# Optimization experiments

Hardware: AMD Instinct MI355X
Metric: run time of the kernel (lower is better)

## Reference

```python
import jax, jax.numpy as jnp
import numpy as np

B, N, C_IN = 8, 2048, 3
D = 64            # graph-conv feature dim
SPARSE_K = 8      # k_neighbors(16) * sparse_ratio(0.5)
LEVELS = 3        # wavelet_levels
H1, H2 = 256, 128 # fusion hidden dims

def _lin(key, fan_in, fan_out):
    k1, k2 = jax.random.split(key)
    s = 1.0 / np.sqrt(fan_in)
    W = jax.random.uniform(k1, (fan_in, fan_out), minval=-s, maxval=s, dtype=jnp.float32)
    b = jax.random.uniform(k2, (fan_out,), minval=-s, maxval=s, dtype=jnp.float32)
    return W, b

def setup_inputs() -> dict:
    key = jax.random.key(0)
    ks = jax.random.split(key, 12)
    x = jax.random.normal(ks[0], (B, N, C_IN), dtype=jnp.float32)
    W1, b1 = _lin(ks[1], C_IN, D)          # feature_transform
    W2, b2 = _lin(ks[2], 2 * D, D)         # edge_conv
    Ws1, bs1 = _lin(ks[3], C_IN, 64)       # suppressor layer 1
    Ws2, bs2 = _lin(ks[4], 64, LEVELS)     # suppressor layer 2
    Wf1, bf1 = _lin(ks[5], D * LEVELS, H1) # fusion
    Wf2, bf2 = _lin(ks[6], H1, H2)
    Wf3, bf3 = _lin(ks[7], H2, C_IN)
    ones = jnp.ones; zeros = jnp.zeros
    return {
        'x': x,
        'W1': W1, 'b1': b1, 'g1': ones((D,), jnp.float32), 'be1': zeros((D,), jnp.float32),
        'W2': W2, 'b2': b2, 'g2': ones((D,), jnp.float32), 'be2': zeros((D,), jnp.float32),
        'Ws1': Ws1, 'bs1': bs1, 'Ws2': Ws2, 'bs2': bs2,
        'Wf1': Wf1, 'bf1': bf1, 'gf1': ones((H1,), jnp.float32), 'bef1': zeros((H1,), jnp.float32),
        'Wf2': Wf2, 'bf2': bf2, 'gf2': ones((H2,), jnp.float32), 'bef2': zeros((H2,), jnp.float32),
        'Wf3': Wf3, 'bf3': bf3,
    }

def _leaky(v):
    return jnp.where(v > 0, v, 0.2 * v)

def reference(x, W1, b1, g1, be1, W2, b2, g2, be2, Ws1, bs1, Ws2, bs2,
              Wf1, bf1, gf1, bef1, Wf2, bf2, gf2, bef2, Wf3, bf3):
    # ---- AdaptiveSparseGraphConv ----
    # feature transform + eval-mode BN (running mean 0 / var 1 -> affine)
    feat = _leaky((x @ W1 + b1) * g1 + be1)                     # [B,N,D]
    # KNN via squared distances (monotonic in true cdist)
    x2 = jnp.sum(x * x, axis=-1)                                # [B,N]
    d2 = x2[:, :, None] + x2[:, None, :] - 2.0 * jnp.einsum('bnc,bmc->bnm', x, x)
    _, idx = jax.lax.top_k(-d2, SPARSE_K)                       # [B,N,k] nearest
    neighbor = jax.vmap(lambda f, i: f[i])(feat, idx)           # [B,N,k,D]
    edge = jnp.concatenate(
        [jnp.broadcast_to(feat[:, :, None, :], neighbor.shape), neighbor], axis=-1)  # [B,N,k,2D]
    conv = _leaky((edge @ W2 + b2) * g2 + be2)                  # [B,N,k,D]
    agg = jnp.max(conv, axis=2)                                 # [B,N,D]
    # ---- AdaptiveFrequencySupressor (per-point wavelet-level weights) ----
    fw = jax.nn.sigmoid(jax.nn.relu(x @ Ws1 + bs1) @ Ws2 + bs2) # [B,N,LEVELS]
    # frequency-adaptive multi-level weighting, concat across levels
    multi = (agg[:, :, None, :] * fw[:, :, :, None]).reshape(B, N, LEVELS * D)  # [B,N,LEVELS*D]
    # ---- EnhancedMultiScaleFusion (eval: dropout off, BN affine) ----
    h = _leaky((multi @ Wf1 + bf1) * gf1 + bef1)
    h = _leaky((h @ Wf2 + bf2) * gf2 + bef2)
    delta = h @ Wf3 + bf3                                       # [B,N,3]
    # ---- residual regularized output ----
    return x + 0.1 * delta
```

## Files before the change

### kernel.cpp

```cpp
#include <hip/hip_runtime.h>
#include <hip/hip_bf16.h>
#include <math.h>

#define BB   8
#define NN   2048
#define BN   16384
#define KNB  8

__device__ __forceinline__ float leaky(float v){ return v > 0.f ? v : 0.2f*v; }

__device__ __forceinline__ ushort f2bf(float f){
    unsigned u = __float_as_uint(f);
    return (ushort)((u + 0x7FFFu + ((u >> 16) & 1u)) >> 16);
}
__device__ __forceinline__ float bf2f(ushort h){
    return __uint_as_float(((unsigned)h) << 16);
}

using bf16x8 = __attribute__((ext_vector_type(8))) short;
using f32x16 = __attribute__((ext_vector_type(16))) float;

__global__ __launch_bounds__(256) void k_pq(
    const float* __restrict__ x,
    const float* __restrict__ W1, const float* __restrict__ b1,
    const float* __restrict__ g1, const float* __restrict__ be1,
    const float* __restrict__ W2,
    const float* __restrict__ Wf1, const float* __restrict__ Wf2,
    float* __restrict__ P, ushort* __restrict__ Qb,
    ushort* __restrict__ Wf1T, ushort* __restrict__ Wf2T)
{
    int t = threadIdx.x;
    int bid = blockIdx.x;
    if (bid >= 256) {
        if (bid < 280) {
            int base = (bid - 256) * 2048 + t * 8;
            #pragma unroll
            for (int j = 0; j < 8; ++j) {
                int e = base + j;
                int n = e / 192, k = e % 192;
                Wf1T[e] = f2bf(Wf1[k*256 + n]);
            }
        } else {
            int base = (bid - 280) * 2048 + t * 8;
            #pragma unroll
            for (int j = 0; j < 8; ++j) {
                int e = base + j;
                int n = e / 256, k = e % 256;
                Wf2T[e] = f2bf(Wf2[k*128 + n]);
            }
        }
        return;
    }

    __shared__ float F_s[64*66];
    __shared__ float W_s[32*132];

    int rb = bid * 64;

    {
        int d = t & 63, g = t >> 6;
        float w0 = W1[d], w1 = W1[64+d], w2 = W1[128+d];
        float bb = b1[d], gg = g1[d], ee = be1[d];
        #pragma unroll 4
        for (int i = 0; i < 16; ++i) {
            int r = g*16 + i;
            const float* xp = &x[(rb + r)*3];
            float f = xp[0]*w0 + xp[1]*w1 + xp[2]*w2 + bb;
            f = leaky(f*gg + ee);
            F_s[r*66 + d] = f;
        }
    }

    int tx = t & 15, ty = t >> 4;
    float acc[4][8];
    #pragma unroll
    for (int i = 0; i < 4; ++i)
        #pragma unroll
        for (int j = 0; j < 8; ++j) acc[i][j] = 0.f;

    for (int k0 = 0; k0 < 64; k0 += 32) {
        __syncthreads();
        #pragma unroll
        for (int it = 0; it < 2; ++it) {
            int i2 = t + it*256;
            int k = i2 >> 4, c8 = (i2 & 15) * 8;
            const float* src = &W2[(k0 + k + (c8 >= 64 ? 64 : 0))*64 + (c8 & 63)];
            *(float4*)&W_s[k*132 + c8]     = *(const float4*)src;
            *(float4*)&W_s[k*132 + c8 + 4] = *(const float4*)(src + 4);
        }
        __syncthreads();
        #pragma unroll 4
        for (int kk = 0; kk < 32; ++kk) {
            float a[4];
            #pragma unroll
            for (int i = 0; i < 4; ++i) a[i] = F_s[(ty*4 + i)*66 + k0 + kk];
            float4 wA = *(const float4*)&W_s[kk*132 + tx*8];
            float4 wB = *(const float4*)&W_s[kk*132 + tx*8 + 4];
            #pragma unroll
            for (int i = 0; i < 4; ++i) {
                acc[i][0] = fmaf(a[i], wA.x, acc[i][0]);
                acc[i][1] = fmaf(a[i], wA.y, acc[i][1]);
                acc[i][2] = fmaf(a[i], wA.z, acc[i][2]);
                acc[i][3] = fmaf(a[i], wA.w, acc[i][3]);
                acc[i][4] = fmaf(a[i], wB.x, acc[i][4]);
                acc[i][5] = fmaf(a[i], wB.y, acc[i][5]);
                acc[i][6] = fmaf(a[i], wB.z, acc[i][6]);
                acc[i][7] = fmaf(a[i], wB.w, acc[i][7]);
            }
        }
    }

    #pragma unroll
    for (int i = 0; i < 4; ++i) {
        int r = rb + ty*4 + i;
        if (tx < 8) {
            *(float4*)&P[r*64 + tx*8]     = make_float4(acc[i][0], acc[i][1], acc[i][2], acc[i][3]);
            *(float4*)&P[r*64 + tx*8 + 4] = make_float4(acc[i][4], acc[i][5], acc[i][6], acc[i][7]);
        } else {
            union { ushort u[8]; uint4 v; } pk;
            #pragma unroll
            for (int j = 0; j < 8; ++j) pk.u[j] = f2bf(acc[i][j]);
            *(uint4*)&Qb[r*64 + (tx - 8)*8] = pk.v;
        }
    }
}

#define CEF(a, b) { float mn_ = fminf(a,b), mx_ = fmaxf(a,b); (a) = mn_; (b) = mx_; }

__global__ __launch_bounds__(1024, 8) void k_knn(const float* __restrict__ x, int* __restrict__ idxo)
{
    __shared__ __align__(16) char smem[51584];
    float4* sp    = (float4*)smem;
    float*  mg    = (float*) (smem + 32768);
    float*  v8buf = (float*) (smem + 49152);
    int*    eqbuf = (int*)   (smem + 49280);
    int*    cnt   = (int*)   (smem + 51328);
    int*    ecnt  = (int*)   (smem + 51456);

    int t = threadIdx.x;
    int b = blockIdx.x >> 6;
    int qbase = (blockIdx.x & 63) * 32;
    int q = t & 31, seg = t >> 5;
    int w = t >> 6, lane = t & 63;

    for (int i = t; i < NN; i += 1024) {
        float a = x[(b*NN + i)*3 + 0];
        float c = x[(b*NN + i)*3 + 1];
        float e = x[(b*NN + i)*3 + 2];
        sp[i] = make_float4(a, c, e, a*a + c*c + e*e);
    }
    __syncthreads();

    float4 qv = sp[qbase + q];
    float R[8];
    #pragma unroll
    for (int j = 0; j < 8; ++j) R[j] = 1e30f;

    int m0 = seg * 64;
    #pragma unroll 2
    for (int g = 0; g < 8; ++g) {
        float S[8];
        #pragma unroll
        for (int jj = 0; jj < 8; ++jj) {
            int m = m0 + g*8 + jj;
            float4 v = sp[m];
            float s = qv.x*v.x; s = fmaf(qv.y, v.y, s); s = fmaf(qv.z, v.z, s);
            float d2 = fmaf(-2.f, s, qv.w + v.w);
            S[jj] = fmaxf(d2, 0.f);
        }
        CEF(S[0],S[1]); CEF(S[2],S[3]); CEF(S[4],S[5]); CEF(S[6],S[7]);
        CEF(S[0],S[2]); CEF(S[1],S[3]); CEF(S[4],S[6]); CEF(S[5],S[7]);
        CEF(S[1],S[2]); CEF(S[5],S[6]);
        CEF(S[0],S[4]); CEF(S[1],S[5]); CEF(S[2],S[6]); CEF(S[3],S[7]);
        CEF(S[2],S[4]); CEF(S[3],S[5]);
        CEF(S[1],S[2]); CEF(S[3],S[4]); CEF(S[5],S[6]);
        #pragma unroll
        for (int j = 0; j < 8; ++j) R[j] = fminf(R[j], S[7-j]);
        CEF(R[0],R[4]); CEF(R[1],R[5]); CEF(R[2],R[6]); CEF(R[3],R[7]);
        CEF(R[0],R[2]); CEF(R[1],R[3]); CEF(R[4],R[6]); CEF(R[5],R[7]);
        CEF(R[0],R[1]); CEF(R[2],R[3]); CEF(R[4],R[5]); CEF(R[6],R[7]);
    }

    {
        float Rp[8];
        #pragma unroll
        for (int j = 0; j < 8; ++j) Rp[j] = __shfl_xor(R[j], 32, 64);
        float C[8];
        #pragma unroll
        for (int j = 0; j < 8; ++j) C[j] = fminf(R[j], Rp[7-j]);
        CEF(C[0],C[4]); CEF(C[1],C[5]); CEF(C[2],C[6]); CEF(C[3],C[7]);
        CEF(C[0],C[2]); CEF(C[1],C[3]); CEF(C[4],C[6]); CEF(C[5],C[7]);
        CEF(C[0],C[1]); CEF(C[2],C[3]); CEF(C[4],C[5]); CEF(C[6],C[7]);
        if (lane < 32) {
            #pragma unroll
            for (int j = 0; j < 8; ++j) mg[(w*32 + lane)*8 + j] = C[j];
        }
    }

    #pragma unroll
    for (int lvl = 0; lvl < 4; ++lvl) {
        int P = 8 >> lvl;
        int sh = 3 - lvl;
        bool active = (t < 32*P);
        float C[8];
        int qq = 0, p = 0;
        __syncthreads();
        if (active) {
            qq = t >> sh; p = t & (P - 1);
            float A[8], Bv[8];
            #pragma unroll
            for (int j = 0; j < 8; ++j) {
                A[j]  = mg[((2*p)*32 + qq)*8 + j];
                Bv[j] = mg[((2*p + 1)*32 + qq)*8 + j];
            }
            #pragma unroll
            for (int j = 0; j < 8; ++j) C[j] = fminf(A[j], Bv[7-j]);
            CEF(C[0],C[4]); CEF(C[1],C[5]); CEF(C[2],C[6]); CEF(C[3],C[7]);
            CEF(C[0],C[2]); CEF(C[1],C[3]); CEF(C[4],C[6]); CEF(C[5],C[7]);
            CEF(C[0],C[1]); CEF(C[2],C[3]); CEF(C[4],C[5]); CEF(C[6],C[7]);
        }
        __syncthreads();
        if (active) {
            if (P > 1) {
                #pragma unroll
                for (int j = 0; j < 8; ++j) mg[(p*32 + qq)*8 + j] = C[j];
            } else {
                v8buf[qq] = C[7];
            }
        }
    }
    if (t >= 32 && t < 64)  cnt[t - 32] = 0;
    if (t >= 64 && t < 96)  ecnt[t - 64] = 0;
    __syncthreads();

    {
        float v8 = v8buf[q];
        int obase = (b*NN + qbase + q)*KNB;
        #pragma unroll 4
        for (int jj = 0; jj < 64; ++jj) {
            int m = m0 + jj;
            float4 v = sp[m];
            float s = qv.x*v.x; s = fmaf(qv.y, v.y, s); s = fmaf(qv.z, v.z, s);
            float d2 = fmaf(-2.f, s, qv.w + v.w);
            d2 = fmaxf(d2, 0.f);
            if (d2 <= v8) {
                if (d2 < v8) {
                    int slot = atomicAdd(&cnt[q], 1);
                    idxo[obase + slot] = b*NN + m;
                } else {
                    int slot = atomicAdd(&ecnt[q], 1);
                    if (slot < 16) eqbuf[q*16 + slot] = m;
                }
            }
        }
    }
    __syncthreads();

    if (t < 32) {
        int qq = t;
        int cLT = cnt[qq];
        int ne = ecnt[qq]; if (ne > 16) ne = 16;
        int need = 8 - cLT;
        int obase = (b*NN + qbase + qq)*KNB;
        for (int k = 0; k < need; ++k) {
            int best = 0x7FFFFFFF, bi = -1;
            for (int i = 0; i < ne; ++i) {
                int v = eqbuf[qq*16 + i];
                if (v < best) { best = v; bi = i; }
            }
            if (bi >= 0) {
                eqbuf[qq*16 + bi] = 0x7FFFFFFF;
                idxo[obase + cLT + k] = b*NN + best;
            }
        }
    }
}

__global__ __launch_bounds__(256) void k_fuse(
    const float* __restrict__ x,
    const float* __restrict__ P, const ushort* __restrict__ Qb,
    const int* __restrict__ idx,
    const float* __restrict__ Ws1, const float* __restrict__ bs1,
    const float* __restrict__ Ws2, const float* __restrict__ bs2,
    const float* __restrict__ b2, const float* __restrict__ g2,
    const float* __restrict__ be2,
    const ushort* __restrict__ Wf1T, const float* __restrict__ bf1,
    const float* __restrict__ gf1, const float* __restrict__ bef1,
    const ushort* __restrict__ Wf2T, const float* __restrict__ bf2,
    const float* __restrict__ gf2, const float* __restrict__ bef2,
    const float* __restrict__ Wf3, const float* __restrict__ bf3,
    float* __restrict__ out)
{
    __shared__ __align__(16) char smem[60928];
    ushort* A_s  = (ushort*)smem;
    ushort* B_s  = (ushort*)(smem + 25600);
    ushort* h1_s = (ushort*)smem;
    ushort* B2_s = (ushort*)(smem + 40960);
    float*  pd   = (float*) (smem + 59392);

    int t = threadIdx.x, w = t >> 6, lane = t & 63;
    int rb = blockIdx.x * 64;

    {
        float ws1a = Ws1[lane], ws1b = Ws1[64+lane], ws1c = Ws1[128+lane];
        float bs1v = bs1[lane];
        float ws2a = Ws2[lane*3+0], ws2b = Ws2[lane*3+1], ws2c = Ws2[lane*3+2];
        float bs20 = bs2[0], bs21 = bs2[1], bs22 = bs2[2];
        float g2v = g2[lane], be2v = be2[lane], b2v = b2[lane];
        for (int i = 0; i < 16; ++i) {
            int r = w*16 + i, p = rb + r;
            float x0 = x[p*3+0], x1 = x[p*3+1], x2 = x[p*3+2];
            float h = fmaxf(fmaf(x2, ws1c, fmaf(x1, ws1b, fmaf(x0, ws1a, bs1v))), 0.f);
            float s0 = h*ws2a, s1 = h*ws2b, s2 = h*ws2c;
            #pragma unroll
            for (int off = 32; off; off >>= 1) {
                s0 += __shfl_xor(s0, off, 64);
                s1 += __shfl_xor(s1, off, 64);
                s2 += __shfl_xor(s2, off, 64);
            }
            float fw0 = 1.f/(1.f + expf(-(s0 + bs20)));
            float fw1 = 1.f/(1.f + expf(-(s1 + bs21)));
            float fw2 = 1.f/(1.f + expf(-(s2 + bs22)));
            float Pv = P[p*64 + lane] + b2v;
            float mx = -1e30f;
            #pragma unroll
            for (int j = 0; j < KNB; ++j) {
                int nb = idx[p*KNB + j];
                float qv = bf2f(Qb[nb*64 + lane]);
                mx = fmaxf(mx, leaky((Pv + qv)*g2v + be2v));
            }
            A_s[r*200 + lane]       = f2bf(mx * fw0);
            A_s[r*200 + 64 + lane]  = f2bf(mx * fw1);
            A_s[r*200 + 128 + lane] = f2bf(mx * fw2);
        }
    }

    int rg = w >> 1;
    int nh = (w & 1) * 128;
    int l31 = lane & 31, kb = (lane >> 5) * 8;
    int row = rg*32 + l31;

    f32x16 acc[4];
    #pragma unroll
    for (int n2 = 0; n2 < 4; ++n2)
        #pragma unroll
        for (int i = 0; i < 16; ++i) acc[n2][i] = 0.f;

    for (int k0 = 0; k0 < 192; k0 += 64) {
        __syncthreads();
        #pragma unroll
        for (int it = 0; it < 8; ++it) {
            int i = t + it*256;
            int n = i >> 3, kq = (i & 7)*8;
            *(uint4*)&B_s[n*72 + kq] = *(const uint4*)&Wf1T[n*192 + k0 + kq];
        }
        __syncthreads();
        #pragma unroll
        for (int s = 0; s < 4; ++s) {
            bf16x8 a = *(const bf16x8*)&A_s[row*200 + k0 + s*16 + kb];
            #pragma unroll
            for (int n2 = 0; n2 < 4; ++n2) {
                bf16x8 b = *(const bf16x8*)&B_s[(nh + n2*32 + l31)*72 + s*16 + kb];
                acc[n2] = __builtin_amdgcn_mfma_f32_32x32x16_bf16(a, b, acc[n2], 0, 0, 0);
            }
        }
    }
    __syncthreads();

    #pragma unroll
    for (int n2 = 0; n2 < 4; ++n2) {
        int c = nh + n2*32 + l31;
        float bv = bf1[c], gv = gf1[c], ev = bef1[c];
        #pragma unroll
        for (int r16 = 0; r16 < 16; ++r16) {
            int rr = (r16 & 3) + 8*(r16 >> 2) + 4*(lane >> 5);
            float v = leaky((acc[n2][r16] + bv)*gv + ev);
            h1_s[(rg*32 + rr)*264 + c] = f2bf(v);
        }
    }

    int ch = (w & 1) * 64;
    f32x16 acc2[2];
    #pragma unroll
    for (int n2 = 0; n2 < 2; ++n2)
        #pragma unroll
        for (int i = 0; i < 16; ++i) acc2[n2][i] = 0.f;

    for (int k0 = 0; k0 < 256; k0 += 64) {
        __syncthreads();
        #pragma unroll
        for (int it = 0; it < 4; ++it) {
            int i = t + it*256;
            int n = i >> 3, kq = (i & 7)*8;
            *(uint4*)&B2_s[n*72 + kq] = *(const uint4*)&Wf2T[n*256 + k0 + kq];
        }
        __syncthreads();
        #pragma unroll
        for (int s = 0; s < 4; ++s) {
            bf16x8 a = *(const bf16x8*)&h1_s[row*264 + k0 + s*16 + kb];
            #pragma unroll
            for (int n2 = 0; n2 < 2; ++n2) {
                bf16x8 b = *(const bf16x8*)&B2_s[(ch + n2*32 + l31)*72 + s*16 + kb];
                acc2[n2] = __builtin_amdgcn_mfma_f32_32x32x16_bf16(a, b, acc2[n2], 0, 0, 0);
            }
        }
    }

    float bv[2], gv[2], ev[2], w3[2][3];
    #pragma unroll
    for (int n2 = 0; n2 < 2; ++n2) {
        int c = ch + n2*32 + l31;
        bv[n2] = bf2[c]; gv[n2] = gf2[c]; ev[n2] = bef2[c];
        #pragma unroll
        for (int l = 0; l < 3; ++l) w3[n2][l] = Wf3[c*3 + l];
    }
    __syncthreads();
    #pragma unroll
    for (int r16 = 0; r16 < 16; ++r16) {
        float d0 = 0.f, d1 = 0.f, d2 = 0.f;
        #pragma unroll
        for (int n2 = 0; n2 < 2; ++n2) {
            float v = leaky((acc2[n2][r16] + bv[n2])*gv[n2] + ev[n2]);
            d0 = fmaf(v, w3[n2][0], d0);
            d1 = fmaf(v, w3[n2][1], d1);
            d2 = fmaf(v, w3[n2][2], d2);
        }
        #pragma unroll
        for (int off = 16; off; off >>= 1) {
            d0 += __shfl_xor(d0, off, 64);
            d1 += __shfl_xor(d1, off, 64);
            d2 += __shfl_xor(d2, off, 64);
        }
        int rr = rg*32 + (r16 & 3) + 8*(r16 >> 2) + 4*(lane >> 5);
        if (l31 < 3) {
            float dl = (l31 == 0) ? d0 : (l31 == 1 ? d1 : d2);
            pd[(rr*2 + (w & 1))*3 + l31] = dl;
        }
    }
    __syncthreads();

    if (t < 192) {
        int r = t / 3, l = t - r*3;
        float delta = pd[(r*2 + 0)*3 + l] + pd[(r*2 + 1)*3 + l] + bf3[l];
        out[(rb + r)*3 + l] = x[(rb + r)*3 + l] + 0.1f*delta;
    }
}

extern "C" void kernel_launch(void* const* d_in, const int* in_sizes, int n_in,
                              void* d_out, int out_size, void* d_ws, size_t ws_size,
                              hipStream_t stream)
{
    const float* x    = (const float*)d_in[0];
    const float* W1   = (const float*)d_in[1];
    const float* b1   = (const float*)d_in[2];
    const float* g1   = (const float*)d_in[3];
    const float* be1  = (const float*)d_in[4];
    const float* W2   = (const float*)d_in[5];
    const float* b2   = (const float*)d_in[6];
    const float* g2   = (const float*)d_in[7];
    const float* be2  = (const float*)d_in[8];
    const float* Ws1  = (const float*)d_in[9];
    const float* bs1  = (const float*)d_in[10];
    const float* Ws2  = (const float*)d_in[11];
    const float* bs2  = (const float*)d_in[12];
    const float* Wf1  = (const float*)d_in[13];
    const float* bf1  = (const float*)d_in[14];
    const float* gf1  = (const float*)d_in[15];
    const float* bef1 = (const float*)d_in[16];
    const float* Wf2  = (const float*)d_in[17];
    const float* bf2  = (const float*)d_in[18];
    const float* gf2  = (const float*)d_in[19];
    const float* bef2 = (const float*)d_in[20];
    const float* Wf3  = (const float*)d_in[21];
    const float* bf3  = (const float*)d_in[22];
    float* out = (float*)d_out;

    char* ws = (char*)d_ws;
    int*    idx   = (int*)   (ws + 0);
    ushort* Wf1T  = (ushort*)(ws + (1u << 20));
    ushort* Wf2T  = (ushort*)(ws + (1u << 20) + (512u << 10));
    float*  P     = (float*) (ws + (2u  << 20));
    ushort* Qb    = (ushort*)(ws + (6u  << 20));

    k_pq<<<296, 256, 0, stream>>>(x, W1, b1, g1, be1, W2, Wf1, Wf2, P, Qb, Wf1T, Wf2T);
    k_knn<<<BB*64, 1024, 0, stream>>>(x, idx);
    k_fuse<<<BN/64, 256, 0, stream>>>(x, P, Qb, idx, Ws1, bs1, Ws2, bs2, b2, g2, be2,
                                      Wf1T, bf1, gf1, bef1, Wf2T, bf2, gf2, bef2,
                                      Wf3, bf3, out);
}
```

Baseline: 163.2 us.

## Merge projection and KNN kernels, shrink fuse tiles to 16 rows with direct-global MFMA

The P/Q projection, weight-transpose and KNN kernels become one 1024-thread launch, with block index ranges selecting the role, so one launch and the gap between the first two stages go away. The fuse kernel now handles 16 rows per block instead of 64, using 16x16x32 MFMAs that read the transposed weights straight from global memory (relying on cache) instead of staging them in shared memory. This cuts LDS use from about 60KB to 9KB and quadruples the block count to raise occupancy. It also prefetches neighbor indices and gathered Q values before the per-point max. The cost is more repeated global and L2 weight traffic and smaller MFMA tiles.

Measured after the change: 157.7 us. 3.3% less time.

```diff
diff --git a/kernel.cpp b/kernel.cpp
--- a/kernel.cpp
+++ b/kernel.cpp
@@ -1,5 +1,4 @@
 #include <hip/hip_runtime.h>
-#include <hip/hip_bf16.h>
 #include <math.h>
 
 #define BB   8
@@ -18,22 +17,87 @@
 }
 
 using bf16x8 = __attribute__((ext_vector_type(8))) short;
-using f32x16 = __attribute__((ext_vector_type(16))) float;
-
-__global__ __launch_bounds__(256) void k_pq(
+using f32x4  = __attribute__((ext_vector_type(4)))  float;
+
+#define CEF(a, b) { float mn_ = fminf(a,b), mx_ = fmaxf(a,b); (a) = mn_; (b) = mx_; }
+
+__global__ __launch_bounds__(1024, 8) void k_front(
     const float* __restrict__ x,
     const float* __restrict__ W1, const float* __restrict__ b1,
     const float* __restrict__ g1, const float* __restrict__ be1,
     const float* __restrict__ W2,
     const float* __restrict__ Wf1, const float* __restrict__ Wf2,
     float* __restrict__ P, ushort* __restrict__ Qb,
-    ushort* __restrict__ Wf1T, ushort* __restrict__ Wf2T)
+    ushort* __restrict__ Wf1T, ushort* __restrict__ Wf2T,
+    int* __restrict__ idxo)
 {
+    __shared__ __align__(16) char smem[51584];
     int t = threadIdx.x;
     int bid = blockIdx.x;
-    if (bid >= 256) {
-        if (bid < 280) {
-            int base = (bid - 256) * 2048 + t * 8;
+
+    if (bid < 256) {
+        float* F_s = (float*)smem;
+        float* W_s = (float*)(smem + 16896);
+        int rb = bid * 64;
+
+        {
+            int d = t & 63, g = t >> 6;
+            float w0 = W1[d], w1 = W1[64+d], w2 = W1[128+d];
+            float bb = b1[d], gg = g1[d], ee = be1[d];
+            #pragma unroll
+            for (int i = 0; i < 4; ++i) {
+                int r = g*4 + i;
+                const float* xp = &x[(rb + r)*3];
+                float f = xp[0]*w0 + xp[1]*w1 + xp[2]*w2 + bb;
+                F_s[r*66 + d] = leaky(f*gg + ee);
+            }
+        }
+
+        int tx = t & 15, ty = t >> 4;
+        float acc[8];
+        #pragma unroll
+        for (int j = 0; j < 8; ++j) acc[j] = 0.f;
+
+        for (int k0 = 0; k0 < 64; k0 += 32) {
+            __syncthreads();
+            {
+                int k = t >> 5, c4 = (t & 31) * 4;
+                const float* src = &W2[(k0 + k + (c4 >= 64 ? 64 : 0))*64 + (c4 & 63)];
+                *(float4*)&W_s[k*132 + c4] = *(const float4*)src;
+            }
+            __syncthreads();
+            #pragma unroll 8
+            for (int kk = 0; kk < 32; ++kk) {
+                float a = F_s[ty*66 + k0 + kk];
+                float4 wA = *(const float4*)&W_s[kk*132 + tx*8];
+                float4 wB = *(const float4*)&W_s[kk*132 + tx*8 + 4];
+                acc[0] = fmaf(a, wA.x, acc[0]);
+                acc[1] = fmaf(a, wA.y, acc[1]);
+                acc[2] = fmaf(a, wA.z, acc[2]);
+                acc[3] = fmaf(a, wA.w, acc[3]);
+                acc[4] = fmaf(a, wB.x, acc[4]);
+                acc[5] = fmaf(a, wB.y, acc[5]);
+                acc[6] = fmaf(a, wB.z, acc[6]);
+                acc[7] = fmaf(a, wB.w, acc[7]);
+            }
+        }
+
+        int r = rb + ty;
+        if (tx < 8) {
+            *(float4*)&P[r*64 + tx*8]     = make_float4(acc[0], acc[1], acc[2], acc[3]);
+            *(float4*)&P[r*64 + tx*8 + 4] = make_float4(acc[4], acc[5], acc[6], acc[7]);
+        } else {
+            union { ushort u[8]; uint4 v; } pk;
+            #pragma unroll
+            for (int j = 0; j < 8; ++j) pk.u[j] = f2bf(acc[j]);
+            *(uint4*)&Qb[r*64 + (tx - 8)*8] = pk.v;
+        }
+        return;
+    }
+
+    if (bid < 266) {
+        if (bid < 262) {
+            int base = (bid - 256) * 8192 + t * 8;
             #pragma unroll
             for (int j = 0; j < 8; ++j) {
                 int e = base + j;
@@ -41,95 +105,17 @@
                 Wf1T[e] = f2bf(Wf1[k*256 + n]);
             }
         } else {
-            int base = (bid - 280) * 2048 + t * 8;
+            int base = (bid - 262) * 8192 + t * 8;
             #pragma unroll
             for (int j = 0; j < 8; ++j) {
                 int e = base + j;
-                int n = e / 256, k = e % 256;
+                int n = e >> 8, k = e & 255;
                 Wf2T[e] = f2bf(Wf2[k*128 + n]);
             }
         }
         return;
     }
 
-    __shared__ float F_s[64*66];
-    __shared__ float W_s[32*132];
-
-    int rb = bid * 64;
-
-    {
-        int d = t & 63, g = t >> 6;
-        float w0 = W1[d], w1 = W1[64+d], w2 = W1[128+d];
-        float bb = b1[d], gg = g1[d], ee = be1[d];
-        #pragma unroll 4
-        for (int i = 0; i < 16; ++i) {
-            int r = g*16 + i;
-            const float* xp = &x[(rb + r)*3];
-            float f = xp[0]*w0 + xp[1]*w1 + xp[2]*w2 + bb;
-            f = leaky(f*gg + ee);
-            F_s[r*66 + d] = f;
-        }
-    }
-
-    int tx = t & 15, ty = t >> 4;
-    float acc[4][8];
-    #pragma unroll
-    for (int i = 0; i < 4; ++i)
-        #pragma unroll
-        for (int j = 0; j < 8; ++j) acc[i][j] = 0.f;
-
-    for (int k0 = 0; k0 < 64; k0 += 32) {
-        __syncthreads();
-        #pragma unroll
-        for (int it = 0; it < 2; ++it) {
-            int i2 = t + it*256;
-            int k = i2 >> 4, c8 = (i2 & 15) * 8;
-            const float* src = &W2[(k0 + k + (c8 >= 64 ? 64 : 0))*64 + (c8 & 63)];
-            *(float4*)&W_s[k*132 + c8]     = *(const float4*)src;
-            *(float4*)&W_s[k*132 + c8 + 4] = *(const float4*)(src + 4);
-        }
-        __syncthreads();
-        #pragma unroll 4
-        for (int kk = 0; kk < 32; ++kk) {
-            float a[4];
-            #pragma unroll
-            for (int i = 0; i < 4; ++i) a[i] = F_s[(ty*4 + i)*66 + k0 + kk];
-            float4 wA = *(const float4*)&W_s[kk*132 + tx*8];
-            float4 wB = *(const float4*)&W_s[kk*132 + tx*8 + 4];
-            #pragma unroll
-            for (int i = 0; i < 4; ++i) {
-                acc[i][0] = fmaf(a[i], wA.x, acc[i][0]);
-                acc[i][1] = fmaf(a[i], wA.y, acc[i][1]);
-                acc[i][2] = fmaf(a[i], wA.z, acc[i][2]);
-                acc[i][3] = fmaf(a[i], wA.w, acc[i][3]);
-                acc[i][4] = fmaf(a[i], wB.x, acc[i][4]);
-                acc[i][5] = fmaf(a[i], wB.y, acc[i][5]);
-                acc[i][6] = fmaf(a[i], wB.z, acc[i][6]);
-                acc[i][7] = fmaf(a[i], wB.w, acc[i][7]);
-            }
-        }
-    }
-
-    #pragma unroll
-    for (int i = 0; i < 4; ++i) {
-        int r = rb + ty*4 + i;
-        if (tx < 8) {
-            *(float4*)&P[r*64 + tx*8]     = make_float4(acc[i][0], acc[i][1], acc[i][2], acc[i][3]);
-            *(float4*)&P[r*64 + tx*8 + 4] = make_float4(acc[i][4], acc[i][5], acc[i][6], acc[i][7]);
-        } else {
-            union { ushort u[8]; uint4 v; } pk;
-            #pragma unroll
-            for (int j = 0; j < 8; ++j) pk.u[j] = f2bf(acc[i][j]);
-            *(uint4*)&Qb[r*64 + (tx - 8)*8] = pk.v;
-        }
-    }
-}
-
-#define CEF(a, b) { float mn_ = fminf(a,b), mx_ = fmaxf(a,b); (a) = mn_; (b) = mx_; }
-
-__global__ __launch_bounds__(1024, 8) void k_knn(const float* __restrict__ x, int* __restrict__ idxo)
-{
-    __shared__ __align__(16) char smem[51584];
     float4* sp    = (float4*)smem;
     float*  mg    = (float*) (smem + 32768);
     float*  v8buf = (float*) (smem + 49152);
@@ -137,9 +123,9 @@
     int*    cnt   = (int*)   (smem + 51328);
     int*    ecnt  = (int*)   (smem + 51456);
 
-    int t = threadIdx.x;
-    int b = blockIdx.x >> 6;
-    int qbase = (blockIdx.x & 63) * 32;
+    int kbid = bid - 266;
+    int b = kbid >> 6;
+    int qbase = (kbid & 63) * 32;
     int q = t & 31, seg = t >> 5;
     int w = t >> 6, lane = t & 63;
 
@@ -199,14 +185,14 @@
 
     #pragma unroll
     for (int lvl = 0; lvl < 4; ++lvl) {
-        int P = 8 >> lvl;
+        int Pn = 8 >> lvl;
         int sh = 3 - lvl;
-        bool active = (t < 32*P);
+        bool active = (t < 32*Pn);
         float C[8];
         int qq = 0, p = 0;
         __syncthreads();
         if (active) {
-            qq = t >> sh; p = t & (P - 1);
+            qq = t >> sh; p = t & (Pn - 1);
             float A[8], Bv[8];
             #pragma unroll
             for (int j = 0; j < 8; ++j) {
@@ -221,7 +207,7 @@
         }
         __syncthreads();
         if (active) {
-            if (P > 1) {
+            if (Pn > 1) {
                 #pragma unroll
                 for (int j = 0; j < 8; ++j) mg[(p*32 + qq)*8 + j] = C[j];
             } else {
@@ -276,7 +262,7 @@
     }
 }
 
-__global__ __launch_bounds__(256) void k_fuse(
+__global__ __launch_bounds__(256, 4) void k_fuse(
     const float* __restrict__ x,
     const float* __restrict__ P, const ushort* __restrict__ Qb,
     const int* __restrict__ idx,
@@ -291,15 +277,14 @@
     const float* __restrict__ Wf3, const float* __restrict__ bf3,
     float* __restrict__ out)
 {
-    __shared__ __align__(16) char smem[60928];
+    __shared__ __align__(16) char smem[9216];
     ushort* A_s  = (ushort*)smem;
-    ushort* B_s  = (ushort*)(smem + 25600);
     ushort* h1_s = (ushort*)smem;
-    ushort* B2_s = (ushort*)(smem + 40960);
-    float*  pd   = (float*) (smem + 59392);
+    float*  pd   = (float*) (smem + 8448);
 
     int t = threadIdx.x, w = t >> 6, lane = t & 63;
-    int rb = blockIdx.x * 64;
+    int rb = blockIdx.x * 16;
+    int l15 = lane & 15, kg = lane >> 4, kb = kg * 8;
 
     {
         float ws1a = Ws1[lane], ws1b = Ws1[64+lane], ws1c = Ws1[128+lane];
@@ -307,8 +292,21 @@
         float ws2a = Ws2[lane*3+0], ws2b = Ws2[lane*3+1], ws2c = Ws2[lane*3+2];
         float bs20 = bs2[0], bs21 = bs2[1], bs22 = bs2[2];
         float g2v = g2[lane], be2v = be2[lane], b2v = b2[lane];
-        for (int i = 0; i < 16; ++i) {
-            int r = w*16 + i, p = rb + r;
+
+        int p0 = rb + w*4;
+        float Pv[4]; int nb[4][8];
+        #pragma unroll
+        for (int i = 0; i < 4; ++i) {
+            Pv[i] = P[(p0 + i)*64 + lane] + b2v;
+            #pragma unroll
+            for (int j = 0; j < 8; ++j) nb[i][j] = idx[(p0 + i)*8 + j];
+        }
+        #pragma unroll
+        for (int i = 0; i < 4; ++i) {
+            int p = p0 + i;
+            float qg[8];
+            #pragma unroll
+            for (int j = 0; j < 8; ++j) qg[j] = bf2f(Qb[nb[i][j]*64 + lane]);
             float x0 = x[p*3+0], x1 = x[p*3+1], x2 = x[p*3+2];
             float h = fmaxf(fmaf(x2, ws1c, fmaf(x1, ws1b, fmaf(x0, ws1a, bs1v))), 0.f);
             float s0 = h*ws2a, s1 = h*ws2b, s2 = h*ws2c;
@@ -321,47 +319,33 @@
             float fw0 = 1.f/(1.f + expf(-(s0 + bs20)));
             float fw1 = 1.f/(1.f + expf(-(s1 + bs21)));
             float fw2 = 1.f/(1.f + expf(-(s2 + bs22)));
-            float Pv = P[p*64 + lane] + b2v;
             float mx = -1e30f;
             #pragma unroll
-            for (int j = 0; j < KNB; ++j) {
-                int nb = idx[p*KNB + j];
-                float qv = bf2f(Qb[nb*64 + lane]);
-                mx = fmaxf(mx, leaky((Pv + qv)*g2v + be2v));
-            }
+            for (int j = 0; j < 8; ++j)
+                mx = fmaxf(mx, leaky((Pv[i] + qg[j])*g2v + be2v));
+            int r = w*4 + i;
             A_s[r*200 + lane]       = f2bf(mx * fw0);
             A_s[r*200 + 64 + lane]  = f2bf(mx * fw1);
             A_s[r*200 + 128 + lane] = f2bf(mx * fw2);
         }
     }
-
-    int rg = w >> 1;
-    int nh = (w & 1) * 128;
-    int l31 = lane & 31, kb = (lane >> 5) * 8;
-    int row = rg*32 + l31;
-
-    f32x16 acc[4];
+    __syncthreads();
+
+    f32x4 acc[4];
     #pragma unroll
     for (int n2 = 0; n2 < 4; ++n2)
         #pragma unroll
-        for (int i = 0; i < 16; ++i) acc[n2][i] = 0.f;
-
-    for (int k0 = 0; k0 < 192; k0 += 64) {
-        __syncthreads();
-        #pragma unroll
-        for (int it = 0; it < 8; ++it) {
-            int i = t + it*256;
-            int n = i >> 3, kq = (i & 7)*8;
-            *(uint4*)&B_s[n*72 + kq] = *(const uint4*)&Wf1T[n*192 + k0 + kq];
-        }
-        __syncthreads();
-        #pragma unroll
-        for (int s = 0; s < 4; ++s) {
-            bf16x8 a = *(const bf16x8*)&A_s[row*200 + k0 + s*16 + kb];
+        for (int i = 0; i < 4; ++i) acc[n2][i] = 0.f;
+
+    {
+        const ushort* Bb = Wf1T + (w*64 + l15)*192 + kb;
+        #pragma unroll
+        for (int k0 = 0; k0 < 192; k0 += 32) {
+            bf16x8 a = *(const bf16x8*)&A_s[l15*200 + k0 + kb];
             #pragma unroll
             for (int n2 = 0; n2 < 4; ++n2) {
-                bf16x8 b = *(const bf16x8*)&B_s[(nh + n2*32 + l31)*72 + s*16 + kb];
-                acc[n2] = __builtin_amdgcn_mfma_f32_32x32x16_bf16(a, b, acc[n2], 0, 0, 0);
+                bf16x8 b = *(const bf16x8*)&Bb[n2*(16*192) + k0];
+                acc[n2] = __builtin_amdgcn_mfma_f32_16x16x32_bf16(a, b, acc[n2], 0, 0, 0);
             }
         }
     }
@@ -369,79 +353,74 @@
 
     #pragma unroll
     for (int n2 = 0; n2 < 4; ++n2) {
-        int c = nh + n2*32 + l31;
+        int c = w*64 + n2*16 + l15;
         float bv = bf1[c], gv = gf1[c], ev = bef1[c];
         #pragma unroll
-        for (int r16 = 0; r16 < 16; ++r16) {
-            int rr = (r16 & 3) + 8*(r16 >> 2) + 4*(lane >> 5);
-            float v = leaky((acc[n2][r16] + bv)*gv + ev);
-            h1_s[(rg*32 + rr)*264 + c] = f2bf(v);
-        }
-    }
-
-    int ch = (w & 1) * 64;
-    f32x16 acc2[2];
+        for (int rg = 0; rg < 4; ++rg) {
+            int r = kg*4 + rg;
+            float v = leaky((acc[n2][rg] + bv)*gv + ev);
+            h1_s[r*264 + c] = f2bf(v);
+        }
+    }
+    __syncthreads();
+
+    f32x4 acc2[2];
     #pragma unroll
     for (int n2 = 0; n2 < 2; ++n2)
         #pragma unroll
-        for (int i = 0; i < 16; ++i) acc2[n2][i] = 0.f;
-
-    for (int k0 = 0; k0 < 256; k0 += 64) {
-        __syncthreads();
-        #pragma unroll
-        for (int it = 0; it < 4; ++it) {
-            int i = t + it*256;
-            int n = i >> 3, kq = (i & 7)*8;
-            *(uint4*)&B2_s[n*72 + kq] = *(const uint4*)&Wf2T[n*256 + k0 + kq];
-        }
-        __syncthreads();
-        #pragma unroll
-        for (int s = 0; s < 4; ++s) {
-            bf16x8 a = *(const bf16x8*)&h1_s[row*264 + k0 + s*16 + kb];
+        for (int i = 0; i < 4; ++i) acc2[n2][i] = 0.f;
+
+    {
+        const ushort* Bb2 = Wf2T + (w*32 + l15)*256 + kb;
+        #pragma unroll
+        for (int k0 = 0; k0 < 256; k0 += 32) {
+            bf16x8 a = *(const bf16x8*)&h1_s[l15*264 + k0 + kb];
             #pragma unroll
             for (int n2 = 0; n2 < 2; ++n2) {
-                bf16x8 b = *(const bf16x8*)&B2_s[(ch + n2*32 + l31)*72 + s*16 + kb];
-                acc2[n2] = __builtin_amdgcn_mfma_f32_32x32x16_bf16(a, b, acc2[n2], 0, 0, 0);
-            }
-        }
-    }
-
-    float bv[2], gv[2], ev[2], w3[2][3];
-    #pragma unroll
-    for (int n2 = 0; n2 < 2; ++n2) {
-        int c = ch + n2*32 + l31;
-        bv[n2] = bf2[c]; gv[n2] = gf2[c]; ev[n2] = bef2[c];
-        #pragma unroll
-        for (int l = 0; l < 3; ++l) w3[n2][l] = Wf3[c*3 + l];
-    }
-    __syncthreads();
-    #pragma unroll
-    for (int r16 = 0; r16 < 16; ++r16) {
-        float d0 = 0.f, d1 = 0.f, d2 = 0.f;
+                bf16x8 b = *(const bf16x8*)&Bb2[n2*(16*256) + k0];
+                acc2[n2] = __builtin_amdgcn_mfma_f32_16x16x32_bf16(a, b, acc2[n2], 0, 0, 0);
+            }
+        }
+    }
+
+    {
+        float bv[2], gv[2], ev[2], w3[2][3];
         #pragma unroll
         for (int n2 = 0; n2 < 2; ++n2) {
-            float v = leaky((acc2[n2][r16] + bv[n2])*gv[n2] + ev[n2]);
-            d0 = fmaf(v, w3[n2][0], d0);
-            d1 = fmaf(v, w3[n2][1], d1);
-            d2 = fmaf(v, w3[n2][2], d2);
-        }
-        #pragma unroll
-        for (int off = 16; off; off >>= 1) {
-            d0 += __shfl_xor(d0, off, 64);
-            d1 += __shfl_xor(d1, off, 64);
-            d2 += __shfl_xor(d2, off, 64);
-        }
-        int rr = rg*32 + (r16 & 3) + 8*(r16 >> 2) + 4*(lane >> 5);
-        if (l31 < 3) {
-            float dl = (l31 == 0) ? d0 : (l31 == 1 ? d1 : d2);
-            pd[(rr*2 + (w & 1))*3 + l31] = dl;
-        }
-    }
-    __syncthreads();
-
-    if (t < 192) {
+            int c = w*32 + n2*16 + l15;
+            bv[n2] = bf2[c]; gv[n2] = gf2[c]; ev[n2] = bef2[c];
+            #pragma unroll
+            for (int l = 0; l < 3; ++l) w3[n2][l] = Wf3[c*3 + l];
+        }
+        #pragma unroll
+        for (int rg = 0; rg < 4; ++rg) {
+            float d0 = 0.f, d1 = 0.f, d2 = 0.f;
+            #pragma unroll
+            for (int n2 = 0; n2 < 2; ++n2) {
+                float v = leaky((acc2[n2][rg] + bv[n2])*gv[n2] + ev[n2]);
+                d0 = fmaf(v, w3[n2][0], d0);
+                d1 = fmaf(v, w3[n2][1], d1);
+                d2 = fmaf(v, w3[n2][2], d2);
+            }
+            #pragma unroll
+            for (int off = 8; off; off >>= 1) {
+                d0 += __shfl_xor(d0, off, 64);
+                d1 += __shfl_xor(d1, off, 64);
+                d2 += __shfl_xor(d2, off, 64);
+            }
+            int r = kg*4 + rg;
+            if (l15 < 3) {
+                float dl = (l15 == 0) ? d0 : (l15 == 1 ? d1 : d2);
+                pd[(r*4 + w)*3 + l15] = dl;
+            }
+        }
+    }
+    __syncthreads();
+
+    if (t < 48) {
         int r = t / 3, l = t - r*3;
-        float delta = pd[(r*2 + 0)*3 + l] + pd[(r*2 + 1)*3 + l] + bf3[l];
+        float delta = pd[(r*4 + 0)*3 + l] + pd[(r*4 + 1)*3 + l]
+                    + pd[(r*4 + 2)*3 + l] + pd[(r*4 + 3)*3 + l] + bf3[l];
         out[(rb + r)*3 + l] = x[(rb + r)*3 + l] + 0.1f*delta;
     }
 }
@@ -482,9 +461,9 @@
     float*  P     = (float*) (ws + (2u  << 20));
     ushort* Qb    = (ushort*)(ws + (6u  << 20));
 
-    k_pq<<<296, 256, 0, stream>>>(x, W1, b1, g1, be1, W2, Wf1, Wf2, P, Qb, Wf1T, Wf2T);
-    k_knn<<<BB*64, 1024, 0, stream>>>(x, idx);
-    k_fuse<<<BN/64, 256, 0, stream>>>(x, P, Qb, idx, Ws1, bs1, Ws2, bs2, b2, g2, be2,
+    k_front<<<778, 1024, 0, stream>>>(x, W1, b1, g1, be1, W2, Wf1, Wf2,
+                                      P, Qb, Wf1T, Wf2T, idx);
+    k_fuse<<<BN/16, 256, 0, stream>>>(x, P, Qb, idx, Ws1, bs1, Ws2, bs2, b2, g2, be2,
                                       Wf1T, bf1, gf1, bef1, Wf2T, bf2, gf2, bef2,
                                       Wf3, bf3, out);
 }
```
